# Kernel tuning notes

Measured on AMD Instinct MI355X. Metric: run time of the kernel, lower is better.

Reference implementation:

```python
import jax, jax.numpy as jnp
import numpy as np

L, I, H = 4, 256, 512          # layers, input_size, hidden_size
SH, LH, GH = 4, 2, 2            # short/long/global heads
NH, HD, FF = SH + LH + GH, H // (SH + LH + GH), 2 * H
S, B = 1024, 8                  # seq (AST nodes), batch
EPS = 1e-5
NEG = -1e9


def _ln(x, g, b):
    m = jnp.mean(x, axis=-1, keepdims=True)
    v = jnp.var(x, axis=-1, keepdims=True)
    return (x - m) * jax.lax.rsqrt(v + EPS) * g + b


def setup_inputs() -> dict:
    key = jax.random.key(0)
    ks = jax.random.split(key, 10)
    w = lambda k, shape: jax.random.normal(k, shape, jnp.float32) * 0.02
    return {
        "nodes": jax.random.normal(ks[0], (S, B, I), jnp.float32),
        "dist": jax.random.randint(ks[1], (B, S, S), 0, 5, jnp.int32),
        "dense_w": w(ks[2], (H, I)), "dense_b": jnp.zeros((H,), jnp.float32),
        "dense_ln_g": jnp.ones((H,), jnp.float32), "dense_ln_b": jnp.zeros((H,), jnp.float32),
        "qkv_w": w(ks[3], (L, 3 * H, H)), "qkv_b": jnp.zeros((L, 3 * H), jnp.float32),
        "out_w": w(ks[4], (L, H, H)), "out_b": jnp.zeros((L, H), jnp.float32),
        "ln1_g": jnp.ones((L, H), jnp.float32), "ln1_b": jnp.zeros((L, H), jnp.float32),
        "ffn_w1": w(ks[5], (L, FF, H)), "ffn_b1": jnp.zeros((L, FF), jnp.float32),
        "ffn_w2": w(ks[6], (L, H, FF)), "ffn_b2": jnp.zeros((L, H), jnp.float32),
        "ln2_g": jnp.ones((L, H), jnp.float32), "ln2_b": jnp.zeros((L, H), jnp.float32),
        "bn_g": jnp.ones((H,), jnp.float32), "bn_b": jnp.zeros((H,), jnp.float32),
    }


def _mask_bias(dist):
    # dist: [B,S,S] int -> additive bias [B,NH,S,S]
    short = (dist == 1)[:, None]                       # [B,1,S,S]
    longm = (dist >= 1)[:, None]
    globm = jnp.broadcast_to((dist[:, 0:1, :] >= 1)[:, None], (dist.shape[0], 1, S, S))
    allowed = jnp.concatenate([
        jnp.broadcast_to(short, (dist.shape[0], SH, S, S)),
        jnp.broadcast_to(longm, (dist.shape[0], LH, S, S)),
        jnp.broadcast_to(globm, (dist.shape[0], GH, S, S)),
    ], axis=1)
    allowed = allowed | jnp.eye(S, dtype=bool)
    return jnp.where(allowed, 0.0, NEG).astype(jnp.float32)


def _forward(nodes, dist, dense_w, dense_b, dense_ln_g, dense_ln_b,
             qkv_w, qkv_b, out_w, out_b, ln1_g, ln1_b,
             ffn_w1, ffn_b1, ffn_w2, ffn_b2, ln2_g, ln2_b, bn_g, bn_b):
    x = jnp.transpose(nodes, (1, 0, 2))                # [B,S,I]
    x = _ln(x @ dense_w.T + dense_b, dense_ln_g, dense_ln_b)  # [B,S,H]
    bias = _mask_bias(dist)                            # [B,NH,S,S]
    scale = 1.0 / np.sqrt(HD)

    def layer(x, p):
        (wqkv, bqkv, wo, bo, g1, b1, w1, bf1, w2, bf2, g2, b2) = p
        qkv = x @ wqkv.T + bqkv                        # [B,S,3H]
        q, k, v = jnp.split(qkv, 3, axis=-1)
        q = q.reshape(B, S, NH, HD).transpose(0, 2, 1, 3)
        k = k.reshape(B, S, NH, HD).transpose(0, 2, 1, 3)
        v = v.reshape(B, S, NH, HD).transpose(0, 2, 1, 3)
        scores = jnp.einsum('bhqd,bhkd->bhqk', q, k) * scale + bias
        attn = jax.nn.softmax(scores, axis=-1)
        o = jnp.einsum('bhqk,bhkd->bhqd', attn, v)
        o = o.transpose(0, 2, 1, 3).reshape(B, S, H) @ wo.T + bo
        x = _ln(x + o, g1, b1)
        f = jax.nn.relu(x @ w1.T + bf1) @ w2.T + bf2
        x = _ln(x + f, g2, b2)
        return x, None

    params = (qkv_w, qkv_b, out_w, out_b, ln1_g, ln1_b,
              ffn_w1, ffn_b1, ffn_w2, ffn_b2, ln2_g, ln2_b)
    x, _ = jax.lax.scan(layer, x, params)
    hidden = x[:, 0]                                   # first token -> [B,H]
    m = jnp.mean(hidden, axis=0)
    v = jnp.var(hidden, axis=0)
    return (hidden - m) * jax.lax.rsqrt(v + EPS) * bn_g + bn_b


def reference(nodes, dist, dense_w, dense_b, dense_ln_g, dense_ln_b,
              qkv_w, qkv_b, out_w, out_b, ln1_g, ln1_b,
              ffn_w1, ffn_b1, ffn_w2, ffn_b2, ln2_g, ln2_b, bn_g, bn_b):
    return _forward(nodes, dist, dense_w, dense_b, dense_ln_g, dense_ln_b,
                    qkv_w, qkv_b, out_w, out_b, ln1_g, ln1_b,
                    ffn_w1, ffn_b1, ffn_w2, ffn_b2, ln2_g, ln2_b, bn_g, bn_b)
```

## Files before the change

### kernel.cpp

```cpp
#include <hip/hip_runtime.h>
#include <hip/hip_bf16.h>
#include <math.h>

#define LAYERS 4
#define IDIM 256
#define HDIM 512
#define NH 8
#define HD 64
#define FF 1024
#define SEQ 1024
#define BATCH 8
#define EPS 1e-5f

typedef __attribute__((ext_vector_type(8))) short short8;
typedef __attribute__((ext_vector_type(4))) short short4v;
typedef __attribute__((ext_vector_type(4))) float f32x4;
typedef __attribute__((ext_vector_type(4))) int int4v;
typedef __attribute__((ext_vector_type(4))) unsigned int uint4v;
typedef unsigned long long u64;

__device__ __forceinline__ short f2bf(float f) {
    unsigned u = __float_as_uint(f);
    u = (u + 0x7FFFu + ((u >> 16) & 1u)) >> 16;
    return (short)u;
}
__device__ __forceinline__ float bf2f(short s) {
    return __uint_as_float(((unsigned)(unsigned short)s) << 16);
}
__device__ __forceinline__ void gll16(const void* g, void* l) {
    __builtin_amdgcn_global_load_lds(
        (const __attribute__((address_space(1))) unsigned int*)g,
        (__attribute__((address_space(3))) unsigned int*)l, 16, 0, 0);
}
__device__ __forceinline__ float fexp2(float x) {
#if __has_builtin(__builtin_amdgcn_exp2f)
    return __builtin_amdgcn_exp2f(x);
#else
    return exp2f(x);
#endif
}

#define CVT_P0 131072u
#define CVT_P1 3276800u
#define CVT_P2 4325376u
#define CVT_P3 6422528u
#define CVT_TOT 8519680u
#define PREP_W 8320
#define PREP_N 2048
__global__ __launch_bounds__(256) void prep_all(
    const float* __restrict__ s0, short* __restrict__ d0,
    const float* __restrict__ s1, short* __restrict__ d1,
    const float* __restrict__ s2, short* __restrict__ d2,
    const float* __restrict__ s3, short* __restrict__ d3,
    const float* __restrict__ s4, short* __restrict__ d4,
    const float* __restrict__ nodes, short* __restrict__ xt,
    const int* __restrict__ dist, u64* __restrict__ mS,
    u64* __restrict__ mL, u64* __restrict__ mG) {
    int blk = blockIdx.x;
    if (blk < PREP_W) {
        size_t i = ((size_t)blk * 256 + threadIdx.x) * 4;
        const float* s; short* d; size_t off;
        if (i < CVT_P0)      { s = s0; d = d0; off = i; }
        else if (i < CVT_P1) { s = s1; d = d1; off = i - CVT_P0; }
        else if (i < CVT_P2) { s = s2; d = d2; off = i - CVT_P1; }
        else if (i < CVT_P3) { s = s3; d = d3; off = i - CVT_P2; }
        else                 { s = s4; d = d4; off = i - CVT_P3; }
        f32x4 f = *(const f32x4*)(s + off);
        short4v o = {f2bf(f[0]), f2bf(f[1]), f2bf(f[2]), f2bf(f[3])};
        *(short4v*)(d + off) = o;
    } else if (blk < PREP_W + PREP_N) {
        size_t idx = ((size_t)(blk - PREP_W) * 256 + threadIdx.x) * 4;
        int i  = idx & (IDIM - 1);
        int sb = idx >> 8;
        int b  = sb & (BATCH - 1);
        int s  = sb >> 3;
        f32x4 f = *(const f32x4*)(nodes + idx);
        short4v o = {f2bf(f[0]), f2bf(f[1]), f2bf(f[2]), f2bf(f[3])};
        *(short4v*)(xt + ((size_t)b * SEQ + s) * IDIM + i) = o;
    } else {
        int blk2 = blk - (PREP_W + PREP_N);
        int b = blk2 >> 10, q = blk2 & 1023;
        int wv = threadIdx.x >> 6, lane = threadIdx.x & 63;
        const int* dp = dist + ((size_t)b * SEQ + q) * SEQ;
        size_t mbase = ((size_t)b * SEQ + q) * 16;
#pragma unroll
        for (int it = 0; it < 4; it++) {
            int w64 = it * 4 + wv;
            int d = dp[w64 * 64 + lane];
            u64 bs = __ballot(d == 1);
            u64 bl = __ballot(d >= 1);
            if (lane == 0) {
                mS[mbase + w64] = bs;
                mL[mbase + w64] = bl;
                if (q == 0) mG[b * 16 + w64] = bl;
            }
        }
    }
}

template<int BM, int BK>
__global__ __launch_bounds__(256, 2)
void gemm_bf16(const short* __restrict__ A, const short* __restrict__ W,
               const float* __restrict__ bias, short* __restrict__ C,
               short* __restrict__ vt, int M, int N, int K, int relu) {
    constexpr int UPR = BK / 8;
    constexpr int RPC = 512 / BK;
    __shared__ __align__(16) short As[BM * BK];
    __shared__ __align__(16) short Ws[128 * BK];
    const int tid = threadIdx.x;
    const int w = tid >> 6, lane = tid & 63;
    const int l15 = lane & 15, quad = lane >> 4;
    const int m0 = blockIdx.y * BM, n0 = blockIdx.x * 128;

    constexpr int NI = (BM == 128) ? 4 : 2;
    const int wm = (BM == 128) ? (w >> 1) * 64 : 0;
    const int wn = (BM == 128) ? (w & 1) * 64 : w * 32;

    f32x4 acc[4][NI];
#pragma unroll
    for (int mi = 0; mi < 4; mi++)
#pragma unroll
        for (int ni = 0; ni < NI; ni++) acc[mi][ni] = (f32x4){0.f, 0.f, 0.f, 0.f};

    const int r_in = (BK == 64) ? (lane >> 3) : (lane >> 4);
    const int c8   = lane & (UPR - 1);

    for (int k0 = 0; k0 < K; k0 += BK) {
#pragma unroll
        for (int rep = 0; rep < BM * BK / 2048; rep++) {
            int chunk = rep * 4 + w;
            int row = chunk * RPC + r_in;
            const short* src = A + (size_t)(m0 + row) * K + k0 + ((c8 ^ (row & (UPR - 1))) << 3);
            gll16(src, (char*)As + chunk * 1024);
        }
#pragma unroll
        for (int rep = 0; rep < 128 * BK / 2048; rep++) {
            int chunk = rep * 4 + w;
            int row = chunk * RPC + r_in;
            const short* src = W + (size_t)(n0 + row) * K + k0 + ((c8 ^ (row & (UPR - 1))) << 3);
            gll16(src, (char*)Ws + chunk * 1024);
        }
        __syncthreads();
#pragma unroll
        for (int ks = 0; ks < BK / 32; ks++) {
            short8 af[4], wf[NI];
            const int dblk = ks * 4 + quad;
#pragma unroll
            for (int mi = 0; mi < 4; mi++) {
                int row = wm + mi * 16 + l15;
                af[mi] = *(const short8*)((const char*)As + row * (BK * 2) + ((dblk ^ (row & (UPR - 1))) << 4));
            }
#pragma unroll
            for (int ni = 0; ni < NI; ni++) {
                int row = wn + ni * 16 + l15;
                wf[ni] = *(const short8*)((const char*)Ws + row * (BK * 2) + ((dblk ^ (row & (UPR - 1))) << 4));
            }
#pragma unroll
            for (int mi = 0; mi < 4; mi++)
#pragma unroll
                for (int ni = 0; ni < NI; ni++)
                    acc[mi][ni] = __builtin_amdgcn_mfma_f32_16x16x32_bf16(
                        af[mi], wf[ni], acc[mi][ni], 0, 0, 0);
        }
        __syncthreads();
    }
    if (vt && n0 >= 1024) {
#pragma unroll
        for (int ni = 0; ni < NI; ni++) {
            int n = n0 + wn + ni * 16 + l15;
            int d = n - 1024, h = d >> 6, dd = d & 63;
            float bz = bias[n];
#pragma unroll
            for (int mi = 0; mi < 4; mi++) {
                int mbase = m0 + wm + mi * 16 + quad * 4;
                int b = mbase >> 10, s = mbase & 1023;
                size_t off = ((size_t)(b * NH + h) * HD + dd) * SEQ + s;
                short4v pk;
#pragma unroll
                for (int r = 0; r < 4; r++) pk[r] = f2bf(acc[mi][ni][r] + bz);
                *(short4v*)(vt + off) = pk;
            }
        }
    } else {
#pragma unroll
        for (int ni = 0; ni < NI; ni++) {
            int n = n0 + wn + ni * 16 + l15;
            float bz = bias[n];
#pragma unroll
            for (int mi = 0; mi < 4; mi++) {
#pragma unroll
                for (int r = 0; r < 4; r++) {
                    int m = m0 + wm + mi * 16 + quad * 4 + r;
                    float v = acc[mi][ni][r] + bz;
                    if (relu) v = fmaxf(v, 0.f);
                    C[(size_t)m * N + n] = f2bf(v);
                }
            }
        }
    }
}

template<int K, bool RES>
__global__ __launch_bounds__(512, 1)
void gemm_ln(const short* __restrict__ A, const short* __restrict__ W,
             const float* __restrict__ bias, const short* __restrict__ resid,
             const float* __restrict__ g, const float* __restrict__ bta,
             short* __restrict__ Y) {
    constexpr int BK = 64, BM = 32, NW = 512, NT = K / BK;
    __shared__ __align__(16) short As[2][BM * BK];
    __shared__ __align__(16) short Ws[2][NW * BK];
    const int tid = threadIdx.x, w = tid >> 6, lane = tid & 63;
    const int l15 = lane & 15, quad = lane >> 4;
    const int m0 = blockIdx.x * BM;
    const int r_in = lane >> 3, c8 = lane & 7;
    const int swz = (c8 ^ r_in) << 3;

    f32x4 acc[2][4];
#pragma unroll
    for (int mi = 0; mi < 2; mi++)
#pragma unroll
        for (int ni = 0; ni < 4; ni++) acc[mi][ni] = (f32x4){0.f, 0.f, 0.f, 0.f};

#define STAGE_LN(bf, k0)                                                          \
    do {                                                                          \
        if (w < 4) {                                                              \
            int row_ = w * 8 + r_in;                                              \
            gll16(A + (size_t)(m0 + row_) * K + (k0) + swz,                       \
                  (char*)As[bf] + w * 1024);                                      \
        }                                                                         \
        _Pragma("unroll")                                                         \
        for (int rep_ = 0; rep_ < 8; rep_++) {                                    \
            int chunk_ = rep_ * 8 + w;                                            \
            int row_ = chunk_ * 8 + r_in;                                         \
            gll16(W + (size_t)row_ * K + (k0) + swz,                              \
                  (char*)Ws[bf] + chunk_ * 1024);                                 \
        }                                                                         \
    } while (0)

    STAGE_LN(0, 0);
    __syncthreads();
    int cur = 0;
    for (int t = 0; t < NT; t++) {
        if (t + 1 < NT) STAGE_LN(cur ^ 1, (t + 1) * BK);
#pragma unroll
        for (int ks = 0; ks < 2; ks++) {
            const int dblk = ks * 4 + quad;
            short8 af[2];
#pragma unroll
            for (int mi = 0; mi < 2; mi++) {
                int row = mi * 16 + l15;
                af[mi] = *(const short8*)((const char*)As[cur] + row * 128 + ((dblk ^ (row & 7)) << 4));
            }
#pragma unroll
            for (int ni = 0; ni < 4; ni++) {
                int row = w * 64 + ni * 16 + l15;
                short8 wf = *(const short8*)((const char*)Ws[cur] + row * 128 + ((dblk ^ (row & 7)) << 4));
#pragma unroll
                for (int mi = 0; mi < 2; mi++)
                    acc[mi][ni] = __builtin_amdgcn_mfma_f32_16x16x32_bf16(
                        wf, af[mi], acc[mi][ni], 0, 0, 0);
            }
        }
        __syncthreads();
        cur ^= 1;
    }
#undef STAGE_LN

    float sum[2] = {0.f, 0.f}, sq[2] = {0.f, 0.f};
#pragma unroll
    for (int mi = 0; mi < 2; mi++)
#pragma unroll
        for (int ni = 0; ni < 4; ni++) {
            int nb = w * 64 + ni * 16 + quad * 4;
            f32x4 bz = *(const f32x4*)(bias + nb);
            f32x4 v;
            if (RES) {
                short4v rv = *(const short4v*)(resid + (size_t)(m0 + mi * 16 + l15) * NW + nb);
#pragma unroll
                for (int r = 0; r < 4; r++) v[r] = acc[mi][ni][r] + bz[r] + bf2f(rv[r]);
            } else {
#pragma unroll
                for (int r = 0; r < 4; r++) v[r] = acc[mi][ni][r] + bz[r];
            }
            acc[mi][ni] = v;
            sum[mi] += v[0] + v[1] + v[2] + v[3];
            sq[mi]  += v[0] * v[0] + v[1] * v[1] + v[2] * v[2] + v[3] * v[3];
        }
#pragma unroll
    for (int mi = 0; mi < 2; mi++) {
        sum[mi] += __shfl_xor(sum[mi], 16); sum[mi] += __shfl_xor(sum[mi], 32);
        sq[mi]  += __shfl_xor(sq[mi], 16);  sq[mi]  += __shfl_xor(sq[mi], 32);
    }
    float* red = (float*)As;
    if (quad == 0) {
#pragma unroll
        for (int mi = 0; mi < 2; mi++) {
            red[(mi * 16 + l15) * 8 + w]       = sum[mi];
            red[256 + (mi * 16 + l15) * 8 + w] = sq[mi];
        }
    }
    __syncthreads();
    float mean[2], inv[2];
#pragma unroll
    for (int mi = 0; mi < 2; mi++) {
        f32x4 s0 = *(const f32x4*)(red + (mi * 16 + l15) * 8);
        f32x4 s1 = *(const f32x4*)(red + (mi * 16 + l15) * 8 + 4);
        f32x4 q0 = *(const f32x4*)(red + 256 + (mi * 16 + l15) * 8);
        f32x4 q1 = *(const f32x4*)(red + 256 + (mi * 16 + l15) * 8 + 4);
        float st = s0[0] + s0[1] + s0[2] + s0[3] + s1[0] + s1[1] + s1[2] + s1[3];
        float qt = q0[0] + q0[1] + q0[2] + q0[3] + q1[0] + q1[1] + q1[2] + q1[3];
        float mn = st * (1.f / NW);
        float vr = qt * (1.f / NW) - mn * mn;
        mean[mi] = mn;
        inv[mi]  = rsqrtf(vr + EPS);
    }
#pragma unroll
    for (int mi = 0; mi < 2; mi++)
#pragma unroll
        for (int ni = 0; ni < 4; ni++) {
            int nb = w * 64 + ni * 16 + quad * 4;
            f32x4 gv = *(const f32x4*)(g + nb);
            f32x4 bv = *(const f32x4*)(bta + nb);
            short4v pk;
#pragma unroll
            for (int r = 0; r < 4; r++)
                pk[r] = f2bf((acc[mi][ni][r] - mean[mi]) * inv[mi] * gv[r] + bv[r]);
            *(short4v*)(Y + (size_t)(m0 + mi * 16 + l15) * NW + nb) = pk;
        }
}

#define EXP2SC 0.18033688011112042f
__global__ __launch_bounds__(256, 4)
void attn_mfma(const short* __restrict__ qkv, const short* __restrict__ vt,
               const u64* __restrict__ maskS, const u64* __restrict__ maskL,
               const u64* __restrict__ maskG, short* __restrict__ out) {
    const int tid = threadIdx.x;
    const int w = tid >> 6, lane = tid & 63, l15 = lane & 15, quad = lane >> 4;
    const int p = blockIdx.x;
    const int g_ = (p & 7) + 8 * (p >> 7);
    const int qt = (p >> 3) & 15;
    const int b = g_ >> 3, h = g_ & 7;
    const int q = qt * 64 + w * 16 + l15;

    __shared__ __align__(16) short Ks[128 * 64];
    __shared__ __align__(16) short Vs[128 * 64];

    short8 qf[2];
    {
        const short* qrow = qkv + ((size_t)(b * SEQ + q) * 1536) + h * 64;
#pragma unroll
        for (int ks = 0; ks < 2; ks++)
            qf[ks] = *(const short8*)(qrow + ks * 32 + quad * 8);
    }
    const u64* mrow = (h < 4) ? (maskS + ((size_t)b * SEQ + q) * 16)
                   : (h < 6) ? (maskL + ((size_t)b * SEQ + q) * 16)
                   :           (maskG + (size_t)b * 16);

    f32x4 of[4];
#pragma unroll
    for (int mt = 0; mt < 4; mt++) of[mt] = (f32x4){0.f, 0.f, 0.f, 0.f};
    float ls0 = 0.f, ls1 = 0.f;

    const int r_in = lane >> 3, c8 = lane & 7;
    const int swz = (c8 ^ r_in) << 3;
    const short* kbase = qkv + ((size_t)b * SEQ) * 1536 + 512 + h * 64 + swz;
    const short* vp = vt + ((size_t)((b * NH + h) * HD) + r_in) * SEQ + swz;
    const int fsw = (l15 & 7);

    for (int kt = 0; kt < SEQ; kt += 128) {
#pragma unroll
        for (int rep = 0; rep < 4; rep++) {
            int c = rep * 4 + w;
            int pr = c * 8 + r_in;
            int pt = pr & 63;
            int key = (pr & 64) | (pt & 32) | (((pt >> 2) & 3) << 3)
                    | (((pt >> 4) & 1) << 2) | (pt & 3);
            gll16(kbase + (size_t)(kt + key) * 1536, (char*)Ks + c * 1024);
        }
#pragma unroll
        for (int rep = 0; rep < 4; rep++) {
            int v = rep * 4 + w;
            gll16(vp + (size_t)((v & 7) * 8) * SEQ + kt + (v >> 3) * 64,
                  (char*)Vs + v * 1024);
        }
        __syncthreads();

#pragma unroll
        for (int t = 0; t < 2; t++) {
            f32x4 sa[4];
#pragma unroll
            for (int g = 0; g < 4; g++) sa[g] = (f32x4){0.f, 0.f, 0.f, 0.f};
#pragma unroll
            for (int ks = 0; ks < 2; ks++) {
                const int dblk = ks * 4 + quad;
#pragma unroll
                for (int g = 0; g < 4; g++) {
                    int row = t * 64 + g * 16 + l15;
                    short8 kf = *(const short8*)((const char*)Ks + row * 128 + ((dblk ^ fsw) << 4));
                    sa[g] = __builtin_amdgcn_mfma_f32_16x16x32_bf16(kf, qf[ks], sa[g], 0, 0, 0);
                }
            }
            u64 mw = mrow[(kt >> 6) + t];
            if ((q >> 6) == (kt >> 6) + t) mw |= 1ull << (q & 63);
            u64 mq2 = mw >> (quad * 8);
            unsigned mlo = (unsigned)mq2, mhi = (unsigned)(mq2 >> 32);
            float pv[4][4];
#pragma unroll
            for (int g = 0; g < 4; g++) {
                unsigned mg = ((g & 2) ? mhi : mlo) >> ((g & 1) * 4);
#pragma unroll
                for (int r = 0; r < 4; r++) {
                    float e = fexp2(sa[g][r] * EXP2SC);
                    e = ((mg >> r) & 1u) ? e : 0.f;
                    pv[g][r] = e;
                    if (g & 1) ls1 += e; else ls0 += e;
                }
            }
            short8 pfrag[2];
#pragma unroll
            for (int g32 = 0; g32 < 2; g32++) {
                uint4v pk;
                pk[0] = __builtin_amdgcn_perm(__float_as_uint(pv[2 * g32][1]),
                                              __float_as_uint(pv[2 * g32][0]), 0x07060302u);
                pk[1] = __builtin_amdgcn_perm(__float_as_uint(pv[2 * g32][3]),
                                              __float_as_uint(pv[2 * g32][2]), 0x07060302u);
                pk[2] = __builtin_amdgcn_perm(__float_as_uint(pv[2 * g32 + 1][1]),
                                              __float_as_uint(pv[2 * g32 + 1][0]), 0x07060302u);
                pk[3] = __builtin_amdgcn_perm(__float_as_uint(pv[2 * g32 + 1][3]),
                                              __float_as_uint(pv[2 * g32 + 1][2]), 0x07060302u);
                pfrag[g32] = __builtin_bit_cast(short8, pk);
            }
#pragma unroll
            for (int g32 = 0; g32 < 2; g32++) {
                const int u = g32 * 4 + quad;
#pragma unroll
                for (int mt = 0; mt < 4; mt++) {
                    int row = mt * 16 + l15;
                    short8 vf = *(const short8*)((const char*)Vs + t * 8192 + row * 128 + ((u ^ fsw) << 4));
                    of[mt] = __builtin_amdgcn_mfma_f32_16x16x32_bf16(vf, pfrag[g32], of[mt], 0, 0, 0);
                }
            }
        }
        __syncthreads();
    }
    float lsum = ls0 + ls1;
    lsum += __shfl_xor(lsum, 16);
    lsum += __shfl_xor(lsum, 32);
    float inv = 1.f / lsum;
#pragma unroll
    for (int mt = 0; mt < 4; mt++) {
        short4v pk;
#pragma unroll
        for (int r = 0; r < 4; r++) pk[r] = f2bf(of[mt][r] * inv);
        *(short4v*)(out + ((size_t)(b * SEQ + q) * HDIM) + h * 64 + mt * 16 + quad * 4) = pk;
    }
}

__global__ __launch_bounds__(256) void final_bn(const short* __restrict__ X,
                                                const float* __restrict__ g,
                                                const float* __restrict__ bb,
                                                float* __restrict__ out) {
    int h = blockIdx.x * 256 + threadIdx.x;
    if (h >= HDIM) return;
    float vals[BATCH];
    float m = 0.f;
#pragma unroll
    for (int b = 0; b < BATCH; b++) {
        vals[b] = bf2f(X[(size_t)b * SEQ * HDIM + h]);
        m += vals[b];
    }
    m *= (1.f / BATCH);
    float v = 0.f;
#pragma unroll
    for (int b = 0; b < BATCH; b++) { float d = vals[b] - m; v += d * d; }
    v *= (1.f / BATCH);
    float inv = rsqrtf(v + EPS);
#pragma unroll
    for (int b = 0; b < BATCH; b++)
        out[b * HDIM + h] = (vals[b] - m) * inv * g[h] + bb[h];
}

extern "C" void kernel_launch(void* const* d_in, const int* in_sizes, int n_in,
                              void* d_out, int out_size, void* d_ws, size_t ws_size,
                              hipStream_t stream) {
    const float* nodes      = (const float*)d_in[0];
    const int*   dist       = (const int*)  d_in[1];
    const float* dense_w    = (const float*)d_in[2];
    const float* dense_b    = (const float*)d_in[3];
    const float* dense_ln_g = (const float*)d_in[4];
    const float* dense_ln_b = (const float*)d_in[5];
    const float* qkv_w      = (const float*)d_in[6];
    const float* qkv_b      = (const float*)d_in[7];
    const float* out_w      = (const float*)d_in[8];
    const float* out_b      = (const float*)d_in[9];
    const float* ln1_g      = (const float*)d_in[10];
    const float* ln1_b      = (const float*)d_in[11];
    const float* ffn_w1     = (const float*)d_in[12];
    const float* ffn_b1     = (const float*)d_in[13];
    const float* ffn_w2     = (const float*)d_in[14];
    const float* ffn_b2     = (const float*)d_in[15];
    const float* ln2_g      = (const float*)d_in[16];
    const float* ln2_b      = (const float*)d_in[17];
    const float* bn_g       = (const float*)d_in[18];
    const float* bn_b       = (const float*)d_in[19];
    float* out = (float*)d_out;

    const int M = BATCH * SEQ;
    const size_t MB = 1024 * 1024;
    char* ws = (char*)d_ws;
    short* Wd   = (short*)(ws + 0 * MB);
    short* Wqkv = (short*)(ws + 1 * MB);
    short* Wo   = (short*)(ws + 9 * MB);
    short* W1   = (short*)(ws + 13 * MB);
    short* W2   = (short*)(ws + 18 * MB);
    u64*   mS   = (u64*)(ws + 23 * MB);
    u64*   mL   = (u64*)(ws + 24 * MB);
    u64*   mG   = (u64*)(ws + 25 * MB);
    short* X    = (short*)(ws + 26 * MB);
    short* QKV  = (short*)(ws + 34 * MB);
    short* Vt   = (short*)(ws + 58 * MB);
    short* AT   = (short*)(ws + 66 * MB);
    short* XT   = QKV;
    short* F1   = QKV;

    prep_all<<<PREP_W + PREP_N + BATCH * SEQ, 256, 0, stream>>>(
        dense_w, Wd, qkv_w, Wqkv, out_w, Wo, ffn_w1, W1, ffn_w2, W2,
        nodes, XT, dist, mS, mL, mG);

    gemm_ln<IDIM, false><<<M / 32, 512, 0, stream>>>(
        XT, Wd, dense_b, nullptr, dense_ln_g, dense_ln_b, X);

    for (int l = 0; l < LAYERS; l++) {
        const short* wqkv = Wqkv + (size_t)l * 3 * HDIM * HDIM;
        const float* bqkv = qkv_b + (size_t)l * 3 * HDIM;
        const short* wo   = Wo + (size_t)l * HDIM * HDIM;
        const float* bo   = out_b + (size_t)l * HDIM;
        const short* w1   = W1 + (size_t)l * FF * HDIM;
        const float* b1   = ffn_b1 + (size_t)l * FF;
        const short* w2   = W2 + (size_t)l * HDIM * FF;
        const float* b2   = ffn_b2 + (size_t)l * HDIM;

        gemm_bf16<128, 64><<<dim3(3 * HDIM / 128, M / 128), 256, 0, stream>>>(
            X, wqkv, bqkv, QKV, Vt, M, 3 * HDIM, HDIM, 0);
        attn_mfma<<<1024, 256, 0, stream>>>(QKV, Vt, mS, mL, mG, AT);
        gemm_ln<HDIM, true><<<M / 32, 512, 0, stream>>>(
            AT, wo, bo, X, ln1_g + l * HDIM, ln1_b + l * HDIM, X);
        gemm_bf16<128, 64><<<dim3(FF / 128, M / 128), 256, 0, stream>>>(
            X, w1, b1, F1, nullptr, M, FF, HDIM, 1);
        gemm_ln<FF, true><<<M / 32, 512, 0, stream>>>(
            F1, w2, b2, X, ln2_g + l * HDIM, ln2_b + l * HDIM, X);
    }
    final_bn<<<(HDIM + 255) / 256, 256, 0, stream>>>(X, bn_g, bn_b, out);
}
```

Baseline: 622.7 us.

## Fuse FFN up-projection, ReLU, down-projection and LayerNorm into one kernel

Replaces the separate FFN1 GEMM and FFN2+LayerNorm kernels with a single kernel per 32-row tile. It keeps the 32x1024 ReLU hidden activations in 128 KB of shared memory, which removes the global write and read of the intermediate F1 buffer. In exchange, each block streams the full W1 and W2 weights with no double buffering, and the large LDS footprint allows only one block per CU. The kernel also reads and writes X in place, which is safe because each block reads its own rows before writing them.

```diff
diff --git a/kernel.cpp b/kernel.cpp
--- a/kernel.cpp
+++ b/kernel.cpp
@@ -329,6 +329,173 @@
         }
 }
 
+__global__ __launch_bounds__(512, 1)
+void fused_ffn(const short* __restrict__ X, const short* __restrict__ W1,
+               const float* __restrict__ b1, const short* __restrict__ W2,
+               const float* __restrict__ b2, const float* __restrict__ g,
+               const float* __restrict__ bta, short* __restrict__ Y) {
+    __shared__ __align__(16) char smem[135168];
+    short* As1 = (short*)smem;
+    char*  W1s = smem + 4096;
+    char*  Hs  = smem;
+    char*  W2s = smem + 65536;
+    float* red = (float*)(smem + 131072);
+
+    const int tid = threadIdx.x, w = tid >> 6, lane = tid & 63;
+    const int l15 = lane & 15, quad = lane >> 4;
+    const int m0 = blockIdx.x * 32;
+    const int r_in = lane >> 3, c8 = lane & 7;
+    const int swz = (c8 ^ r_in) << 3;
+
+    f32x4 acc1[2][8];
+#pragma unroll
+    for (int mi = 0; mi < 2; mi++)
+#pragma unroll
+        for (int ni = 0; ni < 8; ni++) acc1[mi][ni] = (f32x4){0.f, 0.f, 0.f, 0.f};
+
+    for (int t = 0; t < 8; t++) {
+        if (w < 4) {
+            int row = w * 8 + r_in;
+            gll16(X + (size_t)(m0 + row) * HDIM + t * 64 + swz,
+                  (char*)As1 + w * 1024);
+        }
+#pragma unroll
+        for (int rep = 0; rep < 16; rep++) {
+            int c = rep * 8 + w;
+            int row = c * 8 + r_in;
+            gll16(W1 + (size_t)row * HDIM + t * 64 + swz, W1s + c * 1024);
+        }
+        __syncthreads();
+#pragma unroll
+        for (int ks = 0; ks < 2; ks++) {
+            const int dblk = ks * 4 + quad;
+            short8 af[2];
+#pragma unroll
+            for (int mi = 0; mi < 2; mi++) {
+                int row = mi * 16 + l15;
+                af[mi] = *(const short8*)((const char*)As1 + row * 128 + ((dblk ^ (row & 7)) << 4));
+            }
+#pragma unroll
+            for (int ni = 0; ni < 8; ni++) {
+                int row = w * 128 + ni * 16 + l15;
+                short8 wf = *(const short8*)(W1s + row * 128 + ((dblk ^ (row & 7)) << 4));
+#pragma unroll
+                for (int mi = 0; mi < 2; mi++)
+                    acc1[mi][ni] = __builtin_amdgcn_mfma_f32_16x16x32_bf16(
+                        wf, af[mi], acc1[mi][ni], 0, 0, 0);
+            }
+        }
+        __syncthreads();
+    }
+
+#pragma unroll
+    for (int mi = 0; mi < 2; mi++)
+#pragma unroll
+        for (int ni = 0; ni < 8; ni++) {
+            int n = w * 128 + ni * 16 + quad * 4;
+            f32x4 bz = *(const f32x4*)(b1 + n);
+            short4v pk;
+#pragma unroll
+            for (int r = 0; r < 4; r++)
+                pk[r] = f2bf(fmaxf(acc1[mi][ni][r] + bz[r], 0.f));
+            int row = mi * 16 + l15;
+            int u = n >> 3;
+            *(short4v*)(Hs + row * 2048 + ((u ^ (row & 7)) << 4) + (quad & 1) * 8) = pk;
+        }
+
+    f32x4 acc2[2][4];
+#pragma unroll
+    for (int mi = 0; mi < 2; mi++)
+#pragma unroll
+        for (int ni = 0; ni < 4; ni++) acc2[mi][ni] = (f32x4){0.f, 0.f, 0.f, 0.f};
+
+    for (int t2 = 0; t2 < 16; t2++) {
+#pragma unroll
+        for (int rep = 0; rep < 8; rep++) {
+            int c = rep * 8 + w;
+            int row = c * 8 + r_in;
+            gll16(W2 + (size_t)row * FF + t2 * 64 + swz, W2s + c * 1024);
+        }
+        __syncthreads();
+#pragma unroll
+        for (int ks = 0; ks < 2; ks++) {
+            const int dblk = ks * 4 + quad;
+            short8 af[2];
+#pragma unroll
+            for (int mi = 0; mi < 2; mi++) {
+                int row = mi * 16 + l15;
+                af[mi] = *(const short8*)(Hs + row * 2048 + (((t2 * 8 + dblk) ^ (row & 7)) << 4));
+            }
+#pragma unroll
+            for (int ni = 0; ni < 4; ni++) {
+                int row = w * 64 + ni * 16 + l15;
+                short8 wf = *(const short8*)(W2s + row * 128 + ((dblk ^ (row & 7)) << 4));
+#pragma unroll
+                for (int mi = 0; mi < 2; mi++)
+                    acc2[mi][ni] = __builtin_amdgcn_mfma_f32_16x16x32_bf16(
+                        wf, af[mi], acc2[mi][ni], 0, 0, 0);
+            }
+        }
+        __syncthreads();
+    }
+
+    float sum[2] = {0.f, 0.f}, sq[2] = {0.f, 0.f};
+#pragma unroll
+    for (int mi = 0; mi < 2; mi++)
+#pragma unroll
+        for (int ni = 0; ni < 4; ni++) {
+            int nb = w * 64 + ni * 16 + quad * 4;
+            f32x4 bz = *(const f32x4*)(b2 + nb);
+            short4v rv = *(const short4v*)(X + (size_t)(m0 + mi * 16 + l15) * HDIM + nb);
+            f32x4 v;
+#pragma unroll
+            for (int r = 0; r < 4; r++) v[r] = acc2[mi][ni][r] + bz[r] + bf2f(rv[r]);
+            acc2[mi][ni] = v;
+            sum[mi] += v[0] + v[1] + v[2] + v[3];
+            sq[mi]  += v[0] * v[0] + v[1] * v[1] + v[2] * v[2] + v[3] * v[3];
+        }
+#pragma unroll
+    for (int mi = 0; mi < 2; mi++) {
+        sum[mi] += __shfl_xor(sum[mi], 16); sum[mi] += __shfl_xor(sum[mi], 32);
+        sq[mi]  += __shfl_xor(sq[mi], 16);  sq[mi]  += __shfl_xor(sq[mi], 32);
+    }
+    if (quad == 0) {
+#pragma unroll
+        for (int mi = 0; mi < 2; mi++) {
+            red[(mi * 16 + l15) * 8 + w]       = sum[mi];
+            red[256 + (mi * 16 + l15) * 8 + w] = sq[mi];
+        }
+    }
+    __syncthreads();
+    float mean[2], inv[2];
+#pragma unroll
+    for (int mi = 0; mi < 2; mi++) {
+        f32x4 s0 = *(const f32x4*)(red + (mi * 16 + l15) * 8);
+        f32x4 s1 = *(const f32x4*)(red + (mi * 16 + l15) * 8 + 4);
+        f32x4 q0 = *(const f32x4*)(red + 256 + (mi * 16 + l15) * 8);
+        f32x4 q1 = *(const f32x4*)(red + 256 + (mi * 16 + l15) * 8 + 4);
+        float st = s0[0] + s0[1] + s0[2] + s0[3] + s1[0] + s1[1] + s1[2] + s1[3];
+        float qt = q0[0] + q0[1] + q0[2] + q0[3] + q1[0] + q1[1] + q1[2] + q1[3];
+        float mn = st * (1.f / HDIM);
+        float vr = qt * (1.f / HDIM) - mn * mn;
+        mean[mi] = mn;
+        inv[mi]  = rsqrtf(vr + EPS);
+    }
+#pragma unroll
+    for (int mi = 0; mi < 2; mi++)
+#pragma unroll
+        for (int ni = 0; ni < 4; ni++) {
+            int nb = w * 64 + ni * 16 + quad * 4;
+            f32x4 gv = *(const f32x4*)(g + nb);
+            f32x4 bv = *(const f32x4*)(bta + nb);
+            short4v pk;
+#pragma unroll
+            for (int r = 0; r < 4; r++)
+                pk[r] = f2bf((acc2[mi][ni][r] - mean[mi]) * inv[mi] * gv[r] + bv[r]);
+            *(short4v*)(Y + (size_t)(m0 + mi * 16 + l15) * HDIM + nb) = pk;
+        }
+}
+
 #define EXP2SC 0.18033688011112042f
 __global__ __launch_bounds__(256, 4)
 void attn_mfma(const short* __restrict__ qkv, const short* __restrict__ vt,
@@ -521,7 +688,6 @@
     short* Vt   = (short*)(ws + 58 * MB);
     short* AT   = (short*)(ws + 66 * MB);
     short* XT   = QKV;
-    short* F1   = QKV;
 
     prep_all<<<PREP_W + PREP_N + BATCH * SEQ, 256, 0, stream>>>(
         dense_w, Wd, qkv_w, Wqkv, out_w, Wo, ffn_w1, W1, ffn_w2, W2,
@@ -545,10 +711,8 @@
         attn_mfma<<<1024, 256, 0, stream>>>(QKV, Vt, mS, mL, mG, AT);
         gemm_ln<HDIM, true><<<M / 32, 512, 0, stream>>>(
             AT, wo, bo, X, ln1_g + l * HDIM, ln1_b + l * HDIM, X);
-        gemm_bf16<128, 64><<<dim3(FF / 128, M / 128), 256, 0, stream>>>(
-            X, w1, b1, F1, nullptr, M, FF, HDIM, 1);
-        gemm_ln<FF, true><<<M / 32, 512, 0, stream>>>(
-            F1, w2, b2, X, ln2_g + l * HDIM, ln2_b + l * HDIM, X);
+        fused_ffn<<<M / 32, 512, 0, stream>>>(
+            X, w1, b1, w2, b2, ln2_g + l * HDIM, ln2_b + l * HDIM, X);
     }
     final_bn<<<(HDIM + 255) / 256, 256, 0, stream>>>(X, bn_g, bn_b, out);
 }
```

Result: no change. 618.4 us (-0.7%).
